# Optimization experiments

Measured on AMD Instinct MI355X. Metric: run time of the kernel, lower is better.

Reference implementation:

```python
import jax, jax.numpy as jnp
import numpy as np
from jax import lax

D, H, DH, F, K, L, N = 512, 8, 64, 2048, 31, 512, 16
EPS = 1e-5

def layer_norm(x, g, b):
    m = x.mean(-1, keepdims=True)
    v = ((x - m) ** 2).mean(-1, keepdims=True)
    return (x - m) / jnp.sqrt(v + EPS) * g + b

def swish(x):
    return x * jax.nn.sigmoid(x)

def ffn(x, w1, b1, w2, b2):
    return swish(x @ w1.T + b1) @ w2.T + b2

def rel_shift(x):
    # x: (N,H,T,2T-1) -> (N,H,T,T); out[...,i,j] = x[...,i, T-1-i+j]
    T = x.shape[2]
    rows = jnp.arange(T)[:, None]
    cols = (T - 1) - rows + jnp.arange(T)[None, :]
    return x[:, :, rows, cols]

def rel_attn(x, pos_emb, in_w, in_b, out_w, out_b, pos_w, bu, bv):
    Lq, Nb, E = x.shape
    qkv = x @ in_w.T + in_b  # (L,N,3E)
    q, k, v = jnp.split(qkv, 3, axis=-1)
    q = q.reshape(Lq, Nb, H, DH).transpose(1, 2, 0, 3)  # (N,H,L,DH)
    k = k.reshape(Lq, Nb, H, DH).transpose(1, 2, 0, 3)
    v = v.reshape(Lq, Nb, H, DH).transpose(1, 2, 0, 3)
    p = (pos_emb[0] @ pos_w.T).reshape(-1, H, DH).transpose(1, 0, 2)  # (H,2L-1,DH)
    scaling = DH ** -0.5
    q_u = q + bu[None, :, None, :]
    q_v = q + bv[None, :, None, :]
    matrix_ac = jnp.einsum('nhld,nhsd->nhls', q_u, k)        # (N,H,L,L)
    matrix_bd = jnp.einsum('nhld,hmd->nhlm', q_v, p)         # (N,H,L,2L-1)
    matrix_bd = rel_shift(matrix_bd)                         # (N,H,L,L)
    attn = jax.nn.softmax((matrix_ac + matrix_bd) * scaling, axis=-1)
    out = jnp.einsum('nhls,nhsd->nhld', attn, v)
    out = out.transpose(2, 0, 1, 3).reshape(Lq, Nb, E)
    return out @ out_w.T + out_b

def conv_module(x, pw1_w, pw1_b, dw_w, dw_b, g, b, mean, var, pw2_w, pw2_b):
    # x: (L,N,C) -> (N,C,L)
    y = x.transpose(1, 2, 0)
    y = jnp.einsum('ncl,oc->nol', y, pw1_w) + pw1_b[None, :, None]
    a, gate = jnp.split(y, 2, axis=1)
    y = a * jax.nn.sigmoid(gate)  # GLU over channel dim
    pad = (K - 1) // 2
    y = lax.conv_general_dilated(y, dw_w[:, None, :], (1,), [(pad, pad)],
                                 feature_group_count=D,
                                 dimension_numbers=('NCH', 'OIH', 'NCH'))
    y = y + dw_b[None, :, None]
    # BatchNorm1d in eval mode with running stats
    y = (y - mean[None, :, None]) / jnp.sqrt(var[None, :, None] + EPS)
    y = y * g[None, :, None] + b[None, :, None]
    y = swish(y)
    y = jnp.einsum('ncl,oc->nol', y, pw2_w) + pw2_b[None, :, None]
    return y.transpose(2, 0, 1)  # back to (L,N,C)

def setup_inputs() -> dict:
    key = jax.random.key(0)
    ks = iter(jax.random.split(key, 64))
    def nrm(shape, s=0.02):
        return jax.random.normal(next(ks), shape, dtype=jnp.float32) * s
    return {
        'src': jax.random.normal(next(ks), (L, N, D), dtype=jnp.float32),
        'pos_emb': jax.random.normal(next(ks), (1, 2 * L - 1, D), dtype=jnp.float32),
        'ffm_w1': nrm((F, D)), 'ffm_b1': jnp.zeros((F,), jnp.float32),
        'ffm_w2': nrm((D, F)), 'ffm_b2': jnp.zeros((D,), jnp.float32),
        'ff_w1': nrm((F, D)), 'ff_b1': jnp.zeros((F,), jnp.float32),
        'ff_w2': nrm((D, F)), 'ff_b2': jnp.zeros((D,), jnp.float32),
        'in_proj_w': nrm((3 * D, D)), 'in_proj_b': jnp.zeros((3 * D,), jnp.float32),
        'out_proj_w': nrm((D, D)), 'out_proj_b': jnp.zeros((D,), jnp.float32),
        'pos_w': nrm((D, D)),
        'pos_bias_u': nrm((H, DH)), 'pos_bias_v': nrm((H, DH)),
        'conv_pw1_w': nrm((2 * D, D)), 'conv_pw1_b': jnp.zeros((2 * D,), jnp.float32),
        'conv_dw_w': nrm((D, K)), 'conv_dw_b': jnp.zeros((D,), jnp.float32),
        'bn_gamma': jnp.ones((D,), jnp.float32), 'bn_beta': jnp.zeros((D,), jnp.float32),
        'bn_mean': jnp.zeros((D,), jnp.float32), 'bn_var': jnp.ones((D,), jnp.float32),
        'conv_pw2_w': nrm((D, D)), 'conv_pw2_b': jnp.zeros((D,), jnp.float32),
        'ln_ffm_g': jnp.ones((D,), jnp.float32), 'ln_ffm_b': jnp.zeros((D,), jnp.float32),
        'ln_mha_g': jnp.ones((D,), jnp.float32), 'ln_mha_b': jnp.zeros((D,), jnp.float32),
        'ln_conv_g': jnp.ones((D,), jnp.float32), 'ln_conv_b': jnp.zeros((D,), jnp.float32),
        'ln_ff_g': jnp.ones((D,), jnp.float32), 'ln_ff_b': jnp.zeros((D,), jnp.float32),
        'ln_final_g': jnp.ones((D,), jnp.float32), 'ln_final_b': jnp.zeros((D,), jnp.float32),
    }

def reference(src, pos_emb, ffm_w1, ffm_b1, ffm_w2, ffm_b2, ff_w1, ff_b1, ff_w2, ff_b2,
              in_proj_w, in_proj_b, out_proj_w, out_proj_b, pos_w, pos_bias_u, pos_bias_v,
              conv_pw1_w, conv_pw1_b, conv_dw_w, conv_dw_b, bn_gamma, bn_beta, bn_mean, bn_var,
              conv_pw2_w, conv_pw2_b, ln_ffm_g, ln_ffm_b, ln_mha_g, ln_mha_b, ln_conv_g, ln_conv_b,
              ln_ff_g, ln_ff_b, ln_final_g, ln_final_b):
    # pre-norm conformer block, ff_scale = 0.5, dropout omitted (eval)
    x = src
    x = x + 0.5 * ffn(layer_norm(x, ln_ffm_g, ln_ffm_b), ffm_w1, ffm_b1, ffm_w2, ffm_b2)
    x = x + rel_attn(layer_norm(x, ln_mha_g, ln_mha_b), pos_emb,
                     in_proj_w, in_proj_b, out_proj_w, out_proj_b,
                     pos_w, pos_bias_u, pos_bias_v)
    x = x + conv_module(layer_norm(x, ln_conv_g, ln_conv_b),
                        conv_pw1_w, conv_pw1_b, conv_dw_w, conv_dw_b,
                        bn_gamma, bn_beta, bn_mean, bn_var, conv_pw2_w, conv_pw2_b)
    x = x + 0.5 * ffn(layer_norm(x, ln_ff_g, ln_ff_b), ff_w1, ff_b1, ff_w2, ff_b2)
    return layer_norm(x, ln_final_g, ln_final_b)
```

## Files before the change

kernel.cpp:

```cpp
#include <hip/hip_runtime.h>
#include <cstdint>
#include <cstddef>

typedef unsigned short u16;
typedef __attribute__((ext_vector_type(4))) float f32x4;
typedef __attribute__((ext_vector_type(8))) short bf16x8;
typedef __attribute__((ext_vector_type(8))) unsigned short u16x8;

__device__ __forceinline__ float sigm(float x) { return 1.f / (1.f + __expf(-x)); }
__device__ __forceinline__ float bf2f(u16 u) {
    union { unsigned int i; float f; } c; c.i = ((unsigned int)u) << 16; return c.f;
}
__device__ __forceinline__ u16 f2bf(float f) {
    union { float f; unsigned int i; } c; c.f = f;
    unsigned int x = c.i;
    x += 0x7fffu + ((x >> 16) & 1u);
    return (u16)(x >> 16);
}


__global__ void castall_k(const float* __restrict__ s0, const float* __restrict__ s1,
                          const float* __restrict__ s2, const float* __restrict__ s3,
                          const float* __restrict__ s4, const float* __restrict__ s5,
                          const float* __restrict__ s6, const float* __restrict__ s7,
                          const float* __restrict__ s8, const float* __restrict__ s9,
                          u16* __restrict__ dst) {
    int i = (blockIdx.x * 256 + threadIdx.x) << 2;
    if (i >= 6815232) return;
    const float* s; int off;
    if      (i < 1048576) { s = s0; off = 0; }
    else if (i < 2097152) { s = s1; off = 1048576; }
    else if (i < 3145728) { s = s2; off = 2097152; }
    else if (i < 4194304) { s = s3; off = 3145728; }
    else if (i < 4980736) { s = s4; off = 4194304; }
    else if (i < 5242880) { s = s5; off = 4980736; }
    else if (i < 5767168) { s = s6; off = 5242880; }
    else if (i < 6029312) { s = s7; off = 5767168; }
    else if (i < 6291456) { s = s8; off = 6029312; }
    else                  { s = s9; off = 6291456; }
    float4 v = *(const float4*)(s + (i - off));
    union { unsigned int u[2]; } o;
    o.u[0] = (unsigned int)f2bf(v.x) | ((unsigned int)f2bf(v.y) << 16);
    o.u[1] = (unsigned int)f2bf(v.z) | ((unsigned int)f2bf(v.w) << 16);
    *(uint2*)(dst + i) = *(const uint2*)o.u;
}

template <bool OUTBF>
__global__ __launch_bounds__(256) void ln512_k(const float* __restrict__ x,
                                               const float* __restrict__ g,
                                               const float* __restrict__ b,
                                               void* __restrict__ outv) {
    int row = blockIdx.x * 4 + (threadIdx.x >> 6);
    int lane = threadIdx.x & 63;
    const float* xr = x + (size_t)row * 512 + lane * 8;
    float4 v0 = *(const float4*)(xr);
    float4 v1 = *(const float4*)(xr + 4);
    float va[8] = {v0.x, v0.y, v0.z, v0.w, v1.x, v1.y, v1.z, v1.w};
    float s = 0.f;
#pragma unroll
    for (int t = 0; t < 8; t++) s += va[t];
#pragma unroll
    for (int o = 32; o > 0; o >>= 1) s += __shfl_xor(s, o);
    float m = s * (1.0f / 512.0f);
    float q = 0.f;
#pragma unroll
    for (int t = 0; t < 8; t++) { float d = va[t] - m; q += d * d; }
#pragma unroll
    for (int o = 32; o > 0; o >>= 1) q += __shfl_xor(q, o);
    float inv = rsqrtf(q * (1.0f / 512.0f) + 1e-5f);
    int cb = lane * 8;
    if (OUTBF) {
        u16* o = (u16*)outv + (size_t)row * 512 + cb;
#pragma unroll
        for (int t = 0; t < 8; t++)
            o[t] = f2bf((va[t] - m) * inv * g[cb + t] + b[cb + t]);
    } else {
        float* o = (float*)outv + (size_t)row * 512 + cb;
#pragma unroll
        for (int t = 0; t < 8; t++)
            o[t] = (va[t] - m) * inv * g[cb + t] + b[cb + t];
    }
}

__global__ __launch_bounds__(256) void mgemm64_k(
    const u16* __restrict__ A, const u16* __restrict__ B, const float* __restrict__ bias,
    const float* __restrict__ add, void* __restrict__ Cv,
    int M, int Nn, int Kk, float coef, int act, int outbf) {
    __shared__ u16 lA[4][2048];
    __shared__ u16 lB[4][2048];
    int tid = threadIdx.x;
    int lane = tid & 63;
    int w = tid >> 6;
    int quad = lane >> 4, rl = lane & 15;
    int wm = (w >> 1) * 32, wn = (w & 1) * 32;
    int m0 = blockIdx.x << 6, n0 = blockIdx.y << 6;

    f32x4 acc[2][2];
#pragma unroll
    for (int i = 0; i < 2; i++)
#pragma unroll
        for (int j = 0; j < 2; j++) acc[i][j] = (f32x4){0.f, 0.f, 0.f, 0.f};

    int srow = tid >> 2;
    int scol = (tid & 3) << 3;
    const u16* gA = A + (size_t)(m0 + srow) * Kk + scol;
    const u16* gB = B + (size_t)(n0 + srow) * Kk + scol;
    int lso = tid * 8;
    int lra = wm * 32 + rl * 32 + quad * 8;
    int lrb = wn * 32 + rl * 32 + quad * 8;

    auto STAGE2 = [&](int p, int k0) {
#pragma unroll
        for (int s = 0; s < 2; s++) {
            __builtin_amdgcn_global_load_lds(
                (const __attribute__((address_space(1))) void*)(gA + k0 + (s << 5)),
                (__attribute__((address_space(3))) void*)(lA[(p << 1) + s] + lso), 16, 0, 0);
            __builtin_amdgcn_global_load_lds(
                (const __attribute__((address_space(1))) void*)(gB + k0 + (s << 5)),
                (__attribute__((address_space(3))) void*)(lB[(p << 1) + s] + lso), 16, 0, 0);
        }
    };
    auto COMP2 = [&](int p) {
#pragma unroll
        for (int s = 0; s < 2; s++) {
            bf16x8 af[2], bf[2];
#pragma unroll
            for (int t = 0; t < 2; t++) {
                af[t] = *(const bf16x8*)(lA[(p << 1) + s] + lra + t * 512);
                bf[t] = *(const bf16x8*)(lB[(p << 1) + s] + lrb + t * 512);
            }
#pragma unroll
            for (int i = 0; i < 2; i++)
#pragma unroll
                for (int j = 0; j < 2; j++)
                    acc[i][j] = __builtin_amdgcn_mfma_f32_16x16x32_bf16(af[i], bf[j], acc[i][j], 0, 0, 0);
        }
    };

    int nk2 = Kk >> 6;
    STAGE2(0, 0);
    __syncthreads();
    for (int kt = 1; kt < nk2; kt++) {
        STAGE2(kt & 1, kt << 6);
        COMP2((kt - 1) & 1);
        __syncthreads();
    }
    COMP2((nk2 - 1) & 1);

    int rbase = quad * 4;
#pragma unroll
    for (int i = 0; i < 2; i++) {
#pragma unroll
        for (int j = 0; j < 2; j++) {
            int n = n0 + wn + j * 16 + rl;
            float bv = bias ? bias[n] : 0.f;
#pragma unroll
            for (int r = 0; r < 4; r++) {
                int m = m0 + wm + i * 16 + rbase + r;
                float c = acc[i][j][r] + bv;
                if (act == 1) c *= sigm(c);
                size_t o = (size_t)m * Nn + n;
                if (add) c = add[o] + coef * c;
                if (outbf) ((u16*)Cv)[o] = f2bf(c);
                else ((float*)Cv)[o] = c;
            }
        }
    }
}

__global__ __launch_bounds__(256) void mgemmglu_k(
    const u16* __restrict__ A, const u16* __restrict__ B, const float* __restrict__ bias,
    u16* __restrict__ Cv, int Kk) {
    __shared__ u16 lA[4][2048];
    __shared__ u16 lBa[4][2048];
    __shared__ u16 lBg[4][2048];
    int tid = threadIdx.x;
    int lane = tid & 63;
    int w = tid >> 6;
    int quad = lane >> 4, rl = lane & 15;
    int wm = (w >> 1) * 32, wn = (w & 1) * 32;
    int m0 = blockIdx.x << 6, n0 = blockIdx.y << 6;

    f32x4 accA[2][2], accG[2][2];
#pragma unroll
    for (int i = 0; i < 2; i++)
#pragma unroll
        for (int j = 0; j < 2; j++) {
            accA[i][j] = (f32x4){0.f, 0.f, 0.f, 0.f};
            accG[i][j] = (f32x4){0.f, 0.f, 0.f, 0.f};
        }

    int srow = tid >> 2;
    int scol = (tid & 3) << 3;
    const u16* gA  = A + (size_t)(m0 + srow) * Kk + scol;
    const u16* gBa = B + (size_t)(n0 + srow) * Kk + scol;
    const u16* gBg = B + (size_t)(512 + n0 + srow) * Kk + scol;
    int lso = tid * 8;
    int lra = wm * 32 + rl * 32 + quad * 8;
    int lrb = wn * 32 + rl * 32 + quad * 8;

    auto STAGE2 = [&](int p, int k0) {
#pragma unroll
        for (int s = 0; s < 2; s++) {
            __builtin_amdgcn_global_load_lds(
                (const __attribute__((address_space(1))) void*)(gA + k0 + (s << 5)),
                (__attribute__((address_space(3))) void*)(lA[(p << 1) + s] + lso), 16, 0, 0);
            __builtin_amdgcn_global_load_lds(
                (const __attribute__((address_space(1))) void*)(gBa + k0 + (s << 5)),
                (__attribute__((address_space(3))) void*)(lBa[(p << 1) + s] + lso), 16, 0, 0);
            __builtin_amdgcn_global_load_lds(
                (const __attribute__((address_space(1))) void*)(gBg + k0 + (s << 5)),
                (__attribute__((address_space(3))) void*)(lBg[(p << 1) + s] + lso), 16, 0, 0);
        }
    };
    auto COMP2 = [&](int p) {
#pragma unroll
        for (int s = 0; s < 2; s++) {
            bf16x8 af[2], ba[2], bg[2];
#pragma unroll
            for (int t = 0; t < 2; t++) {
                af[t] = *(const bf16x8*)(lA[(p << 1) + s] + lra + t * 512);
                ba[t] = *(const bf16x8*)(lBa[(p << 1) + s] + lrb + t * 512);
                bg[t] = *(const bf16x8*)(lBg[(p << 1) + s] + lrb + t * 512);
            }
#pragma unroll
            for (int i = 0; i < 2; i++)
#pragma unroll
                for (int j = 0; j < 2; j++) {
                    accA[i][j] = __builtin_amdgcn_mfma_f32_16x16x32_bf16(af[i], ba[j], accA[i][j], 0, 0, 0);
                    accG[i][j] = __builtin_amdgcn_mfma_f32_16x16x32_bf16(af[i], bg[j], accG[i][j], 0, 0, 0);
                }
        }
    };

    int nk2 = Kk >> 6;
    STAGE2(0, 0);
    __syncthreads();
    for (int kt = 1; kt < nk2; kt++) {
        STAGE2(kt & 1, kt << 6);
        COMP2((kt - 1) & 1);
        __syncthreads();
    }
    COMP2((nk2 - 1) & 1);

    int rbase = quad * 4;
#pragma unroll
    for (int i = 0; i < 2; i++) {
#pragma unroll
        for (int j = 0; j < 2; j++) {
            int n = n0 + wn + j * 16 + rl;
            float bva = bias[n], bvg = bias[512 + n];
#pragma unroll
            for (int r = 0; r < 4; r++) {
                int m = m0 + wm + i * 16 + rbase + r;
                float a = accA[i][j][r] + bva;
                float g = accG[i][j][r] + bvg;
                Cv[(size_t)m * 512 + n] = f2bf(a * sigm(g));
            }
        }
    }
}

__global__ __launch_bounds__(256) void posb64_k(const u16* __restrict__ A,
                                                const u16* __restrict__ B,
                                                u16* __restrict__ Pbf) {
    __shared__ u16 lA[2][2048];
    __shared__ u16 lB[2][2048];
    const int Kk = 512;
    int tid = threadIdx.x;
    int lane = tid & 63;
    int w = tid >> 6;
    int quad = lane >> 4, rl = lane & 15;
    int wm = (w >> 1) * 32, wn = (w & 1) * 32;
    int m0 = blockIdx.x << 6, n0 = blockIdx.y << 6;

    f32x4 acc[2][2];
#pragma unroll
    for (int i = 0; i < 2; i++)
#pragma unroll
        for (int j = 0; j < 2; j++) acc[i][j] = (f32x4){0.f, 0.f, 0.f, 0.f};

    int srow = tid >> 2;
    int scol = (tid & 3) << 3;
    int ar = m0 + srow; if (ar > 1022) ar = 1022;
    const u16* gA = A + (size_t)ar * Kk + scol;
    const u16* gB = B + (size_t)(n0 + srow) * Kk + scol;
    int lso = tid * 8;
    int lra = wm * 32 + rl * 32 + quad * 8;
    int lrb = wn * 32 + rl * 32 + quad * 8;

    auto STAGE = [&](int buf, int k0) {
        __builtin_amdgcn_global_load_lds(
            (const __attribute__((address_space(1))) void*)(gA + k0),
            (__attribute__((address_space(3))) void*)(lA[buf] + lso), 16, 0, 0);
        __builtin_amdgcn_global_load_lds(
            (const __attribute__((address_space(1))) void*)(gB + k0),
            (__attribute__((address_space(3))) void*)(lB[buf] + lso), 16, 0, 0);
    };
    auto COMP = [&](int buf) {
        bf16x8 af[2], bf[2];
#pragma unroll
        for (int t = 0; t < 2; t++) {
            af[t] = *(const bf16x8*)(lA[buf] + lra + t * 512);
            bf[t] = *(const bf16x8*)(lB[buf] + lrb + t * 512);
        }
#pragma unroll
        for (int i = 0; i < 2; i++)
#pragma unroll
            for (int j = 0; j < 2; j++)
                acc[i][j] = __builtin_amdgcn_mfma_f32_16x16x32_bf16(af[i], bf[j], acc[i][j], 0, 0, 0);
    };

    int nk = Kk >> 5;
    STAGE(0, 0);
    __syncthreads();
    for (int kt = 1; kt < nk; kt++) {
        STAGE(kt & 1, kt << 5);
        COMP((kt - 1) & 1);
        __syncthreads();
    }
    COMP((nk - 1) & 1);

    int rbase = quad * 4;
#pragma unroll
    for (int i = 0; i < 2; i++) {
#pragma unroll
        for (int j = 0; j < 2; j++) {
            int n = n0 + wn + j * 16 + rl;
            int h = n >> 6, d = n & 63;
#pragma unroll
            for (int r = 0; r < 4; r++) {
                int m = m0 + wm + i * 16 + rbase + r;
                u16 val = (m < 1023) ? f2bf(acc[i][j][r]) : (u16)0;
                Pbf[(((size_t)(h * 1024 + m)) << 6) + d] = val;
            }
        }
    }
}

__global__ __launch_bounds__(256) void fattn_k(
    const u16* __restrict__ QU, const u16* __restrict__ QV,
    const u16* __restrict__ Kb, const u16* __restrict__ Pbf,
    const u16* __restrict__ VT, u16* __restrict__ ctx) {
    __shared__ u16 arr[19072];
    u16* sRect = arr;
    u16* sP = arr;
    u16* sCtx = arr + 16768;
    float* sRed = (float*)(arr + 18816);

    int tid = threadIdx.x;
    int lane = tid & 63, w = tid >> 6;
    int quad = lane >> 4, col = lane & 15;
    int nh = blockIdx.x, h = nh & 7, nb = nh >> 3;
    int m0 = blockIdx.y << 5;
    int nlo = 480 - m0;

    const u16* QVz = QV + ((size_t)nh << 15);
    const u16* QUz = QU + ((size_t)nh << 15);
    const u16* Kz  = Kb + ((size_t)nh << 15);
    const u16* Vz  = VT + ((size_t)nh << 15);
    const u16* Pb  = Pbf + ((size_t)h << 16);

    bf16x8 av[2][2];
#pragma unroll
    for (int ks = 0; ks < 2; ks++)
#pragma unroll
        for (int t = 0; t < 2; t++)
            av[ks][t] = *(const bf16x8*)(QVz + ((size_t)(m0 + t * 16 + col) << 6) + (ks << 5) + quad * 8);
#pragma unroll
    for (int idx = 0; idx < 9; idx++) {
        int nt = w + (idx << 2);
        if (nt < 34) {
            int crow = nt * 16 + col;
            const u16* pb = Pb + ((size_t)(nlo + crow) << 6) + quad * 8;
            f32x4 b0 = (f32x4){0.f, 0.f, 0.f, 0.f};
            f32x4 b1 = (f32x4){0.f, 0.f, 0.f, 0.f};
#pragma unroll
            for (int ks = 0; ks < 2; ks++) {
                bf16x8 bfr = *(const bf16x8*)(pb + (ks << 5));
                b0 = __builtin_amdgcn_mfma_f32_16x16x32_bf16(av[ks][0], bfr, b0, 0, 0, 0);
                b1 = __builtin_amdgcn_mfma_f32_16x16x32_bf16(av[ks][1], bfr, b1, 0, 0, 0);
            }
#pragma unroll
            for (int r = 0; r < 4; r++) {
                int ml0 = quad * 4 + r;
                int j0 = crow + ml0 - 31;
                if (j0 >= 0 && j0 < 512) sRect[ml0 * 524 + j0] = f2bf(b0[r]);
                int ml1 = ml0 + 16;
                int j1 = crow + ml1 - 31;
                if (j1 >= 0 && j1 < 512) sRect[ml1 * 524 + j1] = f2bf(b1[r]);
            }
        }
    }

    bf16x8 au[2][2];
#pragma unroll
    for (int ks = 0; ks < 2; ks++)
#pragma unroll
        for (int t = 0; t < 2; t++)
            au[ks][t] = *(const bf16x8*)(QUz + ((size_t)(m0 + t * 16 + col) << 6) + (ks << 5) + quad * 8);
    f32x4 ac[2][8];
#pragma unroll
    for (int t = 0; t < 2; t++)
#pragma unroll
        for (int jt = 0; jt < 8; jt++) ac[t][jt] = (f32x4){0.f, 0.f, 0.f, 0.f};
#pragma unroll
    for (int jt = 0; jt < 8; jt++) {
        const u16* kp = Kz + ((size_t)((w << 7) + jt * 16 + col) << 6) + quad * 8;
#pragma unroll
        for (int ks = 0; ks < 2; ks++) {
            bf16x8 bfr = *(const bf16x8*)(kp + (ks << 5));
            ac[0][jt] = __builtin_amdgcn_mfma_f32_16x16x32_bf16(au[ks][0], bfr, ac[0][jt], 0, 0, 0);
            ac[1][jt] = __builtin_amdgcn_mfma_f32_16x16x32_bf16(au[ks][1], bfr, ac[1][jt], 0, 0, 0);
        }
    }
    __syncthreads();

    float rmax[2][4];
#pragma unroll
    for (int t = 0; t < 2; t++)
#pragma unroll
        for (int r = 0; r < 4; r++) rmax[t][r] = -1e30f;
#pragma unroll
    for (int jt = 0; jt < 8; jt++) {
        int j = (w << 7) + jt * 16 + col;
#pragma unroll
        for (int t = 0; t < 2; t++)
#pragma unroll
            for (int r = 0; r < 4; r++) {
                int ml = t * 16 + quad * 4 + r;
                float v = (ac[t][jt][r] + bf2f(sRect[ml * 524 + j])) * 0.125f;
                ac[t][jt][r] = v;
                rmax[t][r] = fmaxf(rmax[t][r], v);
            }
    }
#pragma unroll
    for (int o = 1; o <= 8; o <<= 1)
#pragma unroll
        for (int t = 0; t < 2; t++)
#pragma unroll
            for (int r = 0; r < 4; r++) rmax[t][r] = fmaxf(rmax[t][r], __shfl_xor(rmax[t][r], o));
    if (col == 0)
#pragma unroll
        for (int t = 0; t < 2; t++)
#pragma unroll
            for (int r = 0; r < 4; r++) sRed[(t * 16 + quad * 4 + r) * 4 + w] = rmax[t][r];
    __syncthreads();
    float gmax[2][4], psum[2][4];
#pragma unroll
    for (int t = 0; t < 2; t++)
#pragma unroll
        for (int r = 0; r < 4; r++) {
            int ml = t * 16 + quad * 4 + r;
            gmax[t][r] = fmaxf(fmaxf(sRed[ml * 4 + 0], sRed[ml * 4 + 1]),
                               fmaxf(sRed[ml * 4 + 2], sRed[ml * 4 + 3]));
            psum[t][r] = 0.f;
        }
    __syncthreads();
#pragma unroll
    for (int jt = 0; jt < 8; jt++)
#pragma unroll
        for (int t = 0; t < 2; t++)
#pragma unroll
            for (int r = 0; r < 4; r++) {
                float e = __expf(ac[t][jt][r] - gmax[t][r]);
                ac[t][jt][r] = e;
                psum[t][r] += e;
            }
#pragma unroll
    for (int o = 1; o <= 8; o <<= 1)
#pragma unroll
        for (int t = 0; t < 2; t++)
#pragma unroll
            for (int r = 0; r < 4; r++) psum[t][r] += __shfl_xor(psum[t][r], o);
    if (col == 0)
#pragma unroll
        for (int t = 0; t < 2; t++)
#pragma unroll
            for (int r = 0; r < 4; r++) sRed[(t * 16 + quad * 4 + r) * 4 + w] = psum[t][r];
    __syncthreads();
    float rinv[2][4];
#pragma unroll
    for (int t = 0; t < 2; t++)
#pragma unroll
        for (int r = 0; r < 4; r++) {
            int ml = t * 16 + quad * 4 + r;
            rinv[t][r] = 1.f / (sRed[ml * 4 + 0] + sRed[ml * 4 + 1] + sRed[ml * 4 + 2] + sRed[ml * 4 + 3]);
        }

#pragma unroll
    for (int jt = 0; jt < 8; jt++) {
        int j = (w << 7) + jt * 16 + col;
#pragma unroll
        for (int t = 0; t < 2; t++)
#pragma unroll
            for (int r = 0; r < 4; r++)
                sP[(t * 16 + quad * 4 + r) * 520 + j] = f2bf(ac[t][jt][r] * rinv[t][r]);
    }
    __syncthreads();

    f32x4 cacc[2];
    cacc[0] = (f32x4){0.f, 0.f, 0.f, 0.f};
    cacc[1] = (f32x4){0.f, 0.f, 0.f, 0.f};
    {
        const u16* vp = Vz + ((size_t)((w << 4) + col) << 9) + quad * 8;
#pragma unroll
        for (int kc = 0; kc < 2; kc++)
#pragma unroll
            for (int s2 = 0; s2 < 8; s2++) {
                int ko = (kc << 8) + (s2 << 5);
                bf16x8 a0 = *(const bf16x8*)(sP + col * 520 + ko + quad * 8);
                bf16x8 a1 = *(const bf16x8*)(sP + (col + 16) * 520 + ko + quad * 8);
                bf16x8 bfr = *(const bf16x8*)(vp + ko);
                cacc[0] = __builtin_amdgcn_mfma_f32_16x16x32_bf16(a0, bfr, cacc[0], 0, 0, 0);
                cacc[1] = __builtin_amdgcn_mfma_f32_16x16x32_bf16(a1, bfr, cacc[1], 0, 0, 0);
            }
    }

#pragma unroll
    for (int t = 0; t < 2; t++)
#pragma unroll
        for (int r = 0; r < 4; r++)
            sCtx[(t * 16 + quad * 4 + r) * 64 + (w << 4) + col] = f2bf(cacc[t][r]);
    __syncthreads();
    {
        int row = tid >> 3, seg = tid & 7;
        u16* dst = ctx + (((size_t)((m0 + row) * 16 + nb)) << 9) + (h << 6) + seg * 8;
        *(uint4*)dst = *(const uint4*)(sCtx + row * 64 + seg * 8);
    }
}

__global__ __launch_bounds__(256) void repack_k(const u16* __restrict__ qkv,
                                                const float* __restrict__ bu,
                                                const float* __restrict__ bv,
                                                u16* __restrict__ QU, u16* __restrict__ QV,
                                                u16* __restrict__ Kb, u16* __restrict__ VT) {
    __shared__ u16 sV[64 * 72];
    int nh = blockIdx.x, h = nh & 7, n = nh >> 3;
    int l0 = blockIdx.y << 6;
    int tid = threadIdx.x;
    int d8 = (tid & 7) << 3;
    float bub[8], bvb[8];
#pragma unroll
    for (int e = 0; e < 8; e++) {
        bub[e] = bu[h * 64 + d8 + e];
        bvb[e] = bv[h * 64 + d8 + e];
    }
#pragma unroll
    for (int rep = 0; rep < 2; rep++) {
        int ll = (tid >> 3) + rep * 32;
        int l = l0 + ll;
        size_t base = (size_t)(l * 16 + n) * 1536 + h * 64 + d8;
        u16x8 q = *(const u16x8*)(qkv + base);
        u16x8 k = *(const u16x8*)(qkv + base + 512);
        u16x8 v = *(const u16x8*)(qkv + base + 1024);
        u16x8 qu, qv;
#pragma unroll
        for (int e = 0; e < 8; e++) {
            float qf = bf2f(q[e]);
            qu[e] = f2bf(qf + bub[e]);
            qv[e] = f2bf(qf + bvb[e]);
        }
        size_t o = ((size_t)nh * 512 + l) * 64 + d8;
        *(u16x8*)(QU + o) = qu;
        *(u16x8*)(QV + o) = qv;
        *(u16x8*)(Kb + o) = k;
        *(u16x8*)(sV + ll * 72 + d8) = v;
    }
    __syncthreads();
    int d = tid >> 2, ls = (tid & 3) << 4;
    u16 tmp[16];
#pragma unroll
    for (int e = 0; e < 16; e++) tmp[e] = sV[(ls + e) * 72 + d];
    u16* dst = VT + ((size_t)nh * 64 + d) * 512 + l0 + ls;
    *(u16x8*)(dst) = *(const u16x8*)(tmp);
    *(u16x8*)(dst + 8) = *(const u16x8*)(tmp + 8);
}

__global__ __launch_bounds__(256) void dwconv_k(
    const u16* __restrict__ g, const float* __restrict__ w, const float* __restrict__ wb,
    const float* __restrict__ bng, const float* __restrict__ bnb, const float* __restrict__ bnm,
    const float* __restrict__ bnv, u16* __restrict__ out) {
    int idx = blockIdx.x * 256 + threadIdx.x;
    int c = idx & 511;
    int t = idx >> 9;
    int n = t & 15, l0 = (t >> 4) << 4;
    float win[46];
#pragma unroll
    for (int q = 0; q < 46; q++) {
        int ll = l0 - 15 + q;
        win[q] = (ll >= 0 && ll < 512) ? bf2f(g[((size_t)(ll * 16 + n) << 9) + c]) : 0.f;
    }
    float wgt[31];
#pragma unroll
    for (int k = 0; k < 31; k++) wgt[k] = w[c * 31 + k];
    float ivg = rsqrtf(bnv[c] + 1e-5f) * bng[c];
    float mc = bnm[c], bc = bnb[c], wbc = wb[c];
#pragma unroll
    for (int r = 0; r < 16; r++) {
        float acc = 0.f;
#pragma unroll
        for (int k = 0; k < 31; k++) acc += wgt[k] * win[r + k];
        acc += wbc;
        float y = (acc - mc) * ivg + bc;
        y = y * sigm(y);
        out[((size_t)((l0 + r) * 16 + n) << 9) + c] = f2bf(y);
    }
}

extern "C" void kernel_launch(void* const* d_in, const int* in_sizes, int n_in,
                              void* d_out, int out_size, void* d_ws, size_t ws_size,
                              hipStream_t stream) {
    const float* src      = (const float*)d_in[0];
    const float* pos_emb  = (const float*)d_in[1];
    const float* ffm_w1   = (const float*)d_in[2];
    const float* ffm_b1   = (const float*)d_in[3];
    const float* ffm_w2   = (const float*)d_in[4];
    const float* ffm_b2   = (const float*)d_in[5];
    const float* ff_w1    = (const float*)d_in[6];
    const float* ff_b1    = (const float*)d_in[7];
    const float* ff_w2    = (const float*)d_in[8];
    const float* ff_b2    = (const float*)d_in[9];
    const float* in_w     = (const float*)d_in[10];
    const float* in_b     = (const float*)d_in[11];
    const float* out_w    = (const float*)d_in[12];
    const float* out_b    = (const float*)d_in[13];
    const float* pos_w    = (const float*)d_in[14];
    const float* bu       = (const float*)d_in[15];
    const float* bv       = (const float*)d_in[16];
    const float* pw1_w    = (const float*)d_in[17];
    const float* pw1_b    = (const float*)d_in[18];
    const float* dw_w     = (const float*)d_in[19];
    const float* dw_b     = (const float*)d_in[20];
    const float* bng      = (const float*)d_in[21];
    const float* bnb      = (const float*)d_in[22];
    const float* bnm      = (const float*)d_in[23];
    const float* bnv      = (const float*)d_in[24];
    const float* pw2_w    = (const float*)d_in[25];
    const float* pw2_b    = (const float*)d_in[26];
    const float* ln_ffm_g = (const float*)d_in[27];
    const float* ln_ffm_b = (const float*)d_in[28];
    const float* ln_mha_g = (const float*)d_in[29];
    const float* ln_mha_b = (const float*)d_in[30];
    const float* ln_cv_g  = (const float*)d_in[31];
    const float* ln_cv_b  = (const float*)d_in[32];
    const float* ln_ff_g  = (const float*)d_in[33];
    const float* ln_ff_b  = (const float*)d_in[34];
    const float* ln_fin_g = (const float*)d_in[35];
    const float* ln_fin_b = (const float*)d_in[36];
    (void)in_sizes; (void)n_in; (void)out_size; (void)ws_size;

    const size_t MEG = 1048576;
    u16* U = (u16*)d_ws;
    float* xA = (float*)U;
    u16* Pbf = U;
    float* xB = (float*)(U + 8 * MEG);
    u16* LNB = U + 16 * MEG;
    u16* BIG = U + 20 * MEG;
    u16* QU = U + 36 * MEG;
    u16* QV = U + 40 * MEG;
    u16* Kb = U + 44 * MEG;
    u16* VT = U + 48 * MEG;
    u16* WB = U + 52 * MEG;
    u16* w_ffm1 = WB;
    u16* w_ffm2 = WB + 1 * MEG;
    u16* w_ff1  = WB + 2 * MEG;
    u16* w_ff2  = WB + 3 * MEG;
    u16* w_in   = WB + 4 * MEG;
    u16* w_out  = WB + 4 * MEG + 786432;
    u16* w_pw1  = WB + 5 * MEG;
    u16* w_pw2  = WB + 5 * MEG + 524288;
    u16* w_pos  = WB + 6029312;
    u16* w_pe   = WB + 6291456;
    u16* CTX = LNB;
    u16* GLU = QU;
    u16* CACT = QV;

    castall_k<<<6656, 256, 0, stream>>>(ffm_w1, ffm_w2, ff_w1, ff_w2, in_w, out_w,
                                        pw1_w, pw2_w, pos_w, pos_emb, WB);

    ln512_k<true><<<2048, 256, 0, stream>>>(src, ln_ffm_g, ln_ffm_b, LNB);
    mgemm64_k<<<dim3(128, 32), 256, 0, stream>>>(LNB, w_ffm1, ffm_b1, nullptr, BIG,
                                                 8192, 2048, 512, 0.f, 1, 1);
    mgemm64_k<<<dim3(128, 8), 256, 0, stream>>>(BIG, w_ffm2, ffm_b2, src, xB,
                                                8192, 512, 2048, 0.5f, 0, 0);

    ln512_k<true><<<2048, 256, 0, stream>>>(xB, ln_mha_g, ln_mha_b, LNB);
    posb64_k<<<dim3(16, 8), 256, 0, stream>>>(w_pe, w_pos, Pbf);
    mgemm64_k<<<dim3(128, 24), 256, 0, stream>>>(LNB, w_in, in_b, nullptr, BIG,
                                                 8192, 1536, 512, 0.f, 0, 1);
    repack_k<<<dim3(128, 8), 256, 0, stream>>>(BIG, bu, bv, QU, QV, Kb, VT);
    fattn_k<<<dim3(128, 16), 256, 0, stream>>>(QU, QV, Kb, Pbf, VT, CTX);
    mgemm64_k<<<dim3(128, 8), 256, 0, stream>>>(CTX, w_out, out_b, xB, xA,
                                                8192, 512, 512, 1.f, 0, 0);

    ln512_k<true><<<2048, 256, 0, stream>>>(xA, ln_cv_g, ln_cv_b, LNB);
    mgemmglu_k<<<dim3(128, 8), 256, 0, stream>>>(LNB, w_pw1, pw1_b, GLU, 512);
    dwconv_k<<<1024, 256, 0, stream>>>(GLU, dw_w, dw_b, bng, bnb, bnm, bnv, CACT);
    mgemm64_k<<<dim3(128, 8), 256, 0, stream>>>(CACT, w_pw2, pw2_b, xA, xB,
                                                8192, 512, 512, 1.f, 0, 0);

    ln512_k<true><<<2048, 256, 0, stream>>>(xB, ln_ff_g, ln_ff_b, LNB);
    mgemm64_k<<<dim3(128, 32), 256, 0, stream>>>(LNB, w_ff1, ff_b1, nullptr, BIG,
                                                 8192, 2048, 512, 0.f, 1, 1);
    mgemm64_k<<<dim3(128, 8), 256, 0, stream>>>(BIG, w_ff2, ff_b2, xB, xA,
                                                8192, 512, 2048, 0.5f, 0, 0);

    ln512_k<false><<<2048, 256, 0, stream>>>(xA, ln_fin_g, ln_fin_b, (float*)d_out);
}
```

Measured before the change: 508.2 us.

## Fuse weight cast with first layernorm, merge QKV and pos GEMMs, add MFMA priority

Merges the weight-cast kernel and the first layernorm into one launch by giving them different block ranges, and folds the positional-projection GEMM into the QKV GEMM as an extra grid row with a dedicated K=64 double-step loop. Also wraps the MFMA loops in the attention kernel with s_setprio to raise wave priority during matrix work. The aim is to cut launch count and tail idle time between small kernels. The risk is branch divergence, and the QKV GEMM's different pipelining may differ in efficiency from the generic mgemm.

Result: no change. 503.9 us (-0.9%).

```diff
diff --git a/kernel.cpp b/kernel.cpp
--- a/kernel.cpp
+++ b/kernel.cpp
@@ -19,30 +19,59 @@
 }
 
 
-__global__ void castall_k(const float* __restrict__ s0, const float* __restrict__ s1,
-                          const float* __restrict__ s2, const float* __restrict__ s3,
-                          const float* __restrict__ s4, const float* __restrict__ s5,
-                          const float* __restrict__ s6, const float* __restrict__ s7,
-                          const float* __restrict__ s8, const float* __restrict__ s9,
-                          u16* __restrict__ dst) {
-    int i = (blockIdx.x * 256 + threadIdx.x) << 2;
-    if (i >= 6815232) return;
-    const float* s; int off;
-    if      (i < 1048576) { s = s0; off = 0; }
-    else if (i < 2097152) { s = s1; off = 1048576; }
-    else if (i < 3145728) { s = s2; off = 2097152; }
-    else if (i < 4194304) { s = s3; off = 3145728; }
-    else if (i < 4980736) { s = s4; off = 4194304; }
-    else if (i < 5242880) { s = s5; off = 4980736; }
-    else if (i < 5767168) { s = s6; off = 5242880; }
-    else if (i < 6029312) { s = s7; off = 5767168; }
-    else if (i < 6291456) { s = s8; off = 6029312; }
-    else                  { s = s9; off = 6291456; }
-    float4 v = *(const float4*)(s + (i - off));
-    union { unsigned int u[2]; } o;
-    o.u[0] = (unsigned int)f2bf(v.x) | ((unsigned int)f2bf(v.y) << 16);
-    o.u[1] = (unsigned int)f2bf(v.z) | ((unsigned int)f2bf(v.w) << 16);
-    *(uint2*)(dst + i) = *(const uint2*)o.u;
+__global__ __launch_bounds__(256) void fusedpre_k(
+    const float* __restrict__ s0, const float* __restrict__ s1,
+    const float* __restrict__ s2, const float* __restrict__ s3,
+    const float* __restrict__ s4, const float* __restrict__ s5,
+    const float* __restrict__ s6, const float* __restrict__ s7,
+    const float* __restrict__ s8, const float* __restrict__ s9,
+    u16* __restrict__ dst,
+    const float* __restrict__ x, const float* __restrict__ g,
+    const float* __restrict__ b, u16* __restrict__ lnout) {
+    if (blockIdx.x < 6656) {
+        int i = (blockIdx.x * 256 + threadIdx.x) << 2;
+        if (i >= 6815232) return;
+        const float* s; int off;
+        if      (i < 1048576) { s = s0; off = 0; }
+        else if (i < 2097152) { s = s1; off = 1048576; }
+        else if (i < 3145728) { s = s2; off = 2097152; }
+        else if (i < 4194304) { s = s3; off = 3145728; }
+        else if (i < 4980736) { s = s4; off = 4194304; }
+        else if (i < 5242880) { s = s5; off = 4980736; }
+        else if (i < 5767168) { s = s6; off = 5242880; }
+        else if (i < 6029312) { s = s7; off = 5767168; }
+        else if (i < 6291456) { s = s8; off = 6029312; }
+        else                  { s = s9; off = 6291456; }
+        float4 v = *(const float4*)(s + (i - off));
+        union { unsigned int u[2]; } o;
+        o.u[0] = (unsigned int)f2bf(v.x) | ((unsigned int)f2bf(v.y) << 16);
+        o.u[1] = (unsigned int)f2bf(v.z) | ((unsigned int)f2bf(v.w) << 16);
+        *(uint2*)(dst + i) = *(const uint2*)o.u;
+    } else {
+        int row = (blockIdx.x - 6656) * 4 + (threadIdx.x >> 6);
+        int lane = threadIdx.x & 63;
+        const float* xr = x + (size_t)row * 512 + lane * 8;
+        float4 v0 = *(const float4*)(xr);
+        float4 v1 = *(const float4*)(xr + 4);
+        float va[8] = {v0.x, v0.y, v0.z, v0.w, v1.x, v1.y, v1.z, v1.w};
+        float s = 0.f;
+#pragma unroll
+        for (int t = 0; t < 8; t++) s += va[t];
+#pragma unroll
+        for (int o = 32; o > 0; o >>= 1) s += __shfl_xor(s, o);
+        float m = s * (1.0f / 512.0f);
+        float q = 0.f;
+#pragma unroll
+        for (int t = 0; t < 8; t++) { float d = va[t] - m; q += d * d; }
+#pragma unroll
+        for (int o = 32; o > 0; o >>= 1) q += __shfl_xor(q, o);
+        float inv = rsqrtf(q * (1.0f / 512.0f) + 1e-5f);
+        int cb = lane * 8;
+        u16* o = lnout + (size_t)row * 512 + cb;
+#pragma unroll
+        for (int t = 0; t < 8; t++)
+            o[t] = f2bf((va[t] - m) * inv * g[cb + t] + b[cb + t]);
+    }
 }
 
 template <bool OUTBF>
@@ -168,6 +197,116 @@
     }
 }
 
+__global__ __launch_bounds__(256) void qkvpos_k(
+    const u16* __restrict__ A, const u16* __restrict__ B, const float* __restrict__ bias,
+    u16* __restrict__ C, const u16* __restrict__ pA, const u16* __restrict__ pB,
+    u16* __restrict__ Pbf) {
+    __shared__ u16 lA[4][2048];
+    __shared__ u16 lB[4][2048];
+    const int Kk = 512;
+    int tid = threadIdx.x;
+    int lane = tid & 63;
+    int w = tid >> 6;
+    int quad = lane >> 4, rl = lane & 15;
+    int wm = (w >> 1) * 32, wn = (w & 1) * 32;
+    int srow = tid >> 2;
+    int scol = (tid & 3) << 3;
+    int lso = tid * 8;
+    int lra = wm * 32 + rl * 32 + quad * 8;
+    int lrb = wn * 32 + rl * 32 + quad * 8;
+
+    f32x4 acc[2][2];
+#pragma unroll
+    for (int i = 0; i < 2; i++)
+#pragma unroll
+        for (int j = 0; j < 2; j++) acc[i][j] = (f32x4){0.f, 0.f, 0.f, 0.f};
+
+    bool ispos = (blockIdx.y == 24);
+    int m0, n0;
+    const u16 *gA, *gB;
+    if (!ispos) {
+        m0 = blockIdx.x << 6; n0 = blockIdx.y << 6;
+        gA = A + (size_t)(m0 + srow) * Kk + scol;
+        gB = B + (size_t)(n0 + srow) * Kk + scol;
+    } else {
+        int bx = blockIdx.x;
+        m0 = (bx >> 3) << 6; n0 = (bx & 7) << 6;
+        int ar = m0 + srow; if (ar > 1022) ar = 1022;
+        gA = pA + (size_t)ar * Kk + scol;
+        gB = pB + (size_t)(n0 + srow) * Kk + scol;
+    }
+
+    auto STAGE2 = [&](int p, int k0) {
+#pragma unroll
+        for (int s = 0; s < 2; s++) {
+            __builtin_amdgcn_global_load_lds(
+                (const __attribute__((address_space(1))) void*)(gA + k0 + (s << 5)),
+                (__attribute__((address_space(3))) void*)(lA[(p << 1) + s] + lso), 16, 0, 0);
+            __builtin_amdgcn_global_load_lds(
+                (const __attribute__((address_space(1))) void*)(gB + k0 + (s << 5)),
+                (__attribute__((address_space(3))) void*)(lB[(p << 1) + s] + lso), 16, 0, 0);
+        }
+    };
+    auto COMP2 = [&](int p) {
+#pragma unroll
+        for (int s = 0; s < 2; s++) {
+            bf16x8 af[2], bf[2];
+#pragma unroll
+            for (int t = 0; t < 2; t++) {
+                af[t] = *(const bf16x8*)(lA[(p << 1) + s] + lra + t * 512);
+                bf[t] = *(const bf16x8*)(lB[(p << 1) + s] + lrb + t * 512);
+            }
+#pragma unroll
+            for (int i = 0; i < 2; i++)
+#pragma unroll
+                for (int j = 0; j < 2; j++)
+                    acc[i][j] = __builtin_amdgcn_mfma_f32_16x16x32_bf16(af[i], bf[j], acc[i][j], 0, 0, 0);
+        }
+    };
+
+    const int nk2 = 8;
+    STAGE2(0, 0);
+    __syncthreads();
+    for (int kt = 1; kt < nk2; kt++) {
+        STAGE2(kt & 1, kt << 6);
+        COMP2((kt - 1) & 1);
+        __syncthreads();
+    }
+    COMP2((nk2 - 1) & 1);
+
+    int rbase = quad * 4;
+    if (!ispos) {
+#pragma unroll
+        for (int i = 0; i < 2; i++) {
+#pragma unroll
+            for (int j = 0; j < 2; j++) {
+                int n = n0 + wn + j * 16 + rl;
+                float bv = bias[n];
+#pragma unroll
+                for (int r = 0; r < 4; r++) {
+                    int m = m0 + wm + i * 16 + rbase + r;
+                    C[(size_t)m * 1536 + n] = f2bf(acc[i][j][r] + bv);
+                }
+            }
+        }
+    } else {
+#pragma unroll
+        for (int i = 0; i < 2; i++) {
+#pragma unroll
+            for (int j = 0; j < 2; j++) {
+                int n = n0 + wn + j * 16 + rl;
+                int h = n >> 6, d = n & 63;
+#pragma unroll
+                for (int r = 0; r < 4; r++) {
+                    int m = m0 + wm + i * 16 + rbase + r;
+                    u16 val = (m < 1023) ? f2bf(acc[i][j][r]) : (u16)0;
+                    Pbf[(((size_t)(h * 1024 + m)) << 6) + d] = val;
+                }
+            }
+        }
+    }
+}
+
 __global__ __launch_bounds__(256) void mgemmglu_k(
     const u16* __restrict__ A, const u16* __restrict__ B, const float* __restrict__ bias,
     u16* __restrict__ Cv, int Kk) {
@@ -261,83 +400,6 @@
     }
 }
 
-__global__ __launch_bounds__(256) void posb64_k(const u16* __restrict__ A,
-                                                const u16* __restrict__ B,
-                                                u16* __restrict__ Pbf) {
-    __shared__ u16 lA[2][2048];
-    __shared__ u16 lB[2][2048];
-    const int Kk = 512;
-    int tid = threadIdx.x;
-    int lane = tid & 63;
-    int w = tid >> 6;
-    int quad = lane >> 4, rl = lane & 15;
-    int wm = (w >> 1) * 32, wn = (w & 1) * 32;
-    int m0 = blockIdx.x << 6, n0 = blockIdx.y << 6;
-
-    f32x4 acc[2][2];
-#pragma unroll
-    for (int i = 0; i < 2; i++)
-#pragma unroll
-        for (int j = 0; j < 2; j++) acc[i][j] = (f32x4){0.f, 0.f, 0.f, 0.f};
-
-    int srow = tid >> 2;
-    int scol = (tid & 3) << 3;
-    int ar = m0 + srow; if (ar > 1022) ar = 1022;
-    const u16* gA = A + (size_t)ar * Kk + scol;
-    const u16* gB = B + (size_t)(n0 + srow) * Kk + scol;
-    int lso = tid * 8;
-    int lra = wm * 32 + rl * 32 + quad * 8;
-    int lrb = wn * 32 + rl * 32 + quad * 8;
-
-    auto STAGE = [&](int buf, int k0) {
-        __builtin_amdgcn_global_load_lds(
-            (const __attribute__((address_space(1))) void*)(gA + k0),
-            (__attribute__((address_space(3))) void*)(lA[buf] + lso), 16, 0, 0);
-        __builtin_amdgcn_global_load_lds(
-            (const __attribute__((address_space(1))) void*)(gB + k0),
-            (__attribute__((address_space(3))) void*)(lB[buf] + lso), 16, 0, 0);
-    };
-    auto COMP = [&](int buf) {
-        bf16x8 af[2], bf[2];
-#pragma unroll
-        for (int t = 0; t < 2; t++) {
-            af[t] = *(const bf16x8*)(lA[buf] + lra + t * 512);
-            bf[t] = *(const bf16x8*)(lB[buf] + lrb + t * 512);
-        }
-#pragma unroll
-        for (int i = 0; i < 2; i++)
-#pragma unroll
-            for (int j = 0; j < 2; j++)
-                acc[i][j] = __builtin_amdgcn_mfma_f32_16x16x32_bf16(af[i], bf[j], acc[i][j], 0, 0, 0);
-    };
-
-    int nk = Kk >> 5;
-    STAGE(0, 0);
-    __syncthreads();
-    for (int kt = 1; kt < nk; kt++) {
-        STAGE(kt & 1, kt << 5);
-        COMP((kt - 1) & 1);
-        __syncthreads();
-    }
-    COMP((nk - 1) & 1);
-
-    int rbase = quad * 4;
-#pragma unroll
-    for (int i = 0; i < 2; i++) {
-#pragma unroll
-        for (int j = 0; j < 2; j++) {
-            int n = n0 + wn + j * 16 + rl;
-            int h = n >> 6, d = n & 63;
-#pragma unroll
-            for (int r = 0; r < 4; r++) {
-                int m = m0 + wm + i * 16 + rbase + r;
-                u16 val = (m < 1023) ? f2bf(acc[i][j][r]) : (u16)0;
-                Pbf[(((size_t)(h * 1024 + m)) << 6) + d] = val;
-            }
-        }
-    }
-}
-
 __global__ __launch_bounds__(256) void fattn_k(
     const u16* __restrict__ QU, const u16* __restrict__ QV,
     const u16* __restrict__ Kb, const u16* __restrict__ Pbf,
@@ -367,6 +429,7 @@
 #pragma unroll
         for (int t = 0; t < 2; t++)
             av[ks][t] = *(const bf16x8*)(QVz + ((size_t)(m0 + t * 16 + col) << 6) + (ks << 5) + quad * 8);
+    __builtin_amdgcn_s_setprio(1);
 #pragma unroll
     for (int idx = 0; idx < 9; idx++) {
         int nt = w + (idx << 2);
@@ -392,6 +455,7 @@
             }
         }
     }
+    __builtin_amdgcn_s_setprio(0);
 
     bf16x8 au[2][2];
 #pragma unroll
@@ -404,6 +468,7 @@
     for (int t = 0; t < 2; t++)
 #pragma unroll
         for (int jt = 0; jt < 8; jt++) ac[t][jt] = (f32x4){0.f, 0.f, 0.f, 0.f};
+    __builtin_amdgcn_s_setprio(1);
 #pragma unroll
     for (int jt = 0; jt < 8; jt++) {
         const u16* kp = Kz + ((size_t)((w << 7) + jt * 16 + col) << 6) + quad * 8;
@@ -414,6 +479,7 @@
             ac[1][jt] = __builtin_amdgcn_mfma_f32_16x16x32_bf16(au[ks][1], bfr, ac[1][jt], 0, 0, 0);
         }
     }
+    __builtin_amdgcn_s_setprio(0);
     __syncthreads();
 
     float rmax[2][4];
@@ -504,6 +570,7 @@
     cacc[1] = (f32x4){0.f, 0.f, 0.f, 0.f};
     {
         const u16* vp = Vz + ((size_t)((w << 4) + col) << 9) + quad * 8;
+        __builtin_amdgcn_s_setprio(1);
 #pragma unroll
         for (int kc = 0; kc < 2; kc++)
 #pragma unroll
@@ -515,6 +582,7 @@
                 cacc[0] = __builtin_amdgcn_mfma_f32_16x16x32_bf16(a0, bfr, cacc[0], 0, 0, 0);
                 cacc[1] = __builtin_amdgcn_mfma_f32_16x16x32_bf16(a1, bfr, cacc[1], 0, 0, 0);
             }
+        __builtin_amdgcn_s_setprio(0);
     }
 
 #pragma unroll
@@ -676,19 +744,18 @@
     u16* GLU = QU;
     u16* CACT = QV;
 
-    castall_k<<<6656, 256, 0, stream>>>(ffm_w1, ffm_w2, ff_w1, ff_w2, in_w, out_w,
-                                        pw1_w, pw2_w, pos_w, pos_emb, WB);
-
-    ln512_k<true><<<2048, 256, 0, stream>>>(src, ln_ffm_g, ln_ffm_b, LNB);
+    fusedpre_k<<<8704, 256, 0, stream>>>(ffm_w1, ffm_w2, ff_w1, ff_w2, in_w, out_w,
+                                         pw1_w, pw2_w, pos_w, pos_emb, WB,
+                                         src, ln_ffm_g, ln_ffm_b, LNB);
+
     mgemm64_k<<<dim3(128, 32), 256, 0, stream>>>(LNB, w_ffm1, ffm_b1, nullptr, BIG,
                                                  8192, 2048, 512, 0.f, 1, 1);
     mgemm64_k<<<dim3(128, 8), 256, 0, stream>>>(BIG, w_ffm2, ffm_b2, src, xB,
                                                 8192, 512, 2048, 0.5f, 0, 0);
 
     ln512_k<true><<<2048, 256, 0, stream>>>(xB, ln_mha_g, ln_mha_b, LNB);
-    posb64_k<<<dim3(16, 8), 256, 0, stream>>>(w_pe, w_pos, Pbf);
-    mgemm64_k<<<dim3(128, 24), 256, 0, stream>>>(LNB, w_in, in_b, nullptr, BIG,
-                                                 8192, 1536, 512, 0.f, 0, 1);
+    qkvpos_k<<<dim3(128, 25), 256, 0, stream>>>(LNB, w_in, in_b, BIG,
+                                                w_pe, w_pos, Pbf);
     repack_k<<<dim3(128, 8), 256, 0, stream>>>(BIG, bu, bv, QU, QV, Kb, VT);
     fattn_k<<<dim3(128, 16), 256, 0, stream>>>(QU, QV, Kb, Pbf, VT, CTX);
     mgemm64_k<<<dim3(128, 8), 256, 0, stream>>>(CTX, w_out, out_b, xB, xA,
```
